# Optimization experiments

Hardware: AMD Instinct MI355X
Metric: run time of the kernel (lower is better)

## Reference

```python
import jax, jax.numpy as jnp
import numpy as np

P, N, M = 4, 8192, 8192

def setup_inputs() -> dict:
    key = jax.random.key(0)
    k1, k2, k3, k4, k5 = jax.random.split(key, 5)
    return {
        "camera_pts": jax.random.normal(k1, (P, N, 3), dtype=jnp.float32),
        "cad_pts": jax.random.normal(k2, (P, M, 3), dtype=jnp.float32),
        "part_weight": jax.random.uniform(k3, (P,), dtype=jnp.float32),
        "rot_quat": jax.random.normal(k4, (P, 4), dtype=jnp.float32),
        "tra": jax.random.normal(k5, (P, 3, 1), dtype=jnp.float32),
    }

def _quat_to_rot(q):
    # q: [P,4] in (w,x,y,z) order, normalized outside
    a, b, c, d = q[:, 0], q[:, 1], q[:, 2], q[:, 3]
    rows = jnp.stack([
        1 - 2*c*c - 2*d*d, 2*b*c - 2*a*d,     2*a*c + 2*b*d,
        2*b*c + 2*a*d,     1 - 2*b*b - 2*d*d, 2*c*d - 2*a*b,
        2*b*d - 2*a*c,     2*a*b + 2*c*d,     1 - 2*b*b - 2*c*c,
    ], axis=-1)  # [P,9]
    return rows.reshape(-1, 3, 3)

def _chamfer(x, y):
    # x: [N,4], y: [M,4] -> scalar bidirectional chamfer (Euclidean, not squared)
    x2 = jnp.sum(x * x, axis=-1)              # [N]
    y2 = jnp.sum(y * y, axis=-1)              # [M]
    d2 = x2[:, None] + y2[None, :] - 2.0 * (x @ y.T)
    dist = jnp.sqrt(jnp.clip(d2, 0.0))        # [N,M]
    return jnp.mean(jnp.min(dist, axis=1)) + jnp.mean(jnp.min(dist, axis=0))

def reference(camera_pts, cad_pts, part_weight, rot_quat, tra):
    q = rot_quat / jnp.linalg.norm(rot_quat, axis=1, keepdims=True)
    rot = _quat_to_rot(q)                                       # [P,3,3]
    top = jnp.concatenate([rot, tra], axis=2)                   # [P,3,4]
    bottom = jnp.broadcast_to(jnp.array([[[0.0, 0.0, 0.0, 1.0]]], dtype=rot.dtype), (rot.shape[0], 1, 4))
    transforms = jnp.concatenate([top, bottom], axis=1)         # [P,4,4]
    ones_cad = jnp.ones(cad_pts.shape[:-1] + (1,), dtype=cad_pts.dtype)
    ones_cam = jnp.ones(camera_pts.shape[:-1] + (1,), dtype=camera_pts.dtype)
    cad_h = jnp.concatenate([cad_pts, ones_cad], axis=-1)       # [P,M,4]
    cam_h = jnp.concatenate([camera_pts, ones_cam], axis=-1)    # [P,N,4]
    cad_base = jnp.einsum('pij,pmj->pmi', transforms, cad_h)    # [P,M,4]
    cd = jax.vmap(_chamfer)(cad_base, cam_h)                    # [P]
    all_objective = jnp.sum(part_weight * cd)
    return all_objective, jax.lax.stop_gradient(transforms)
```

## Files before the change

kernel.cpp:

```cpp
#include <hip/hip_runtime.h>
#include <math.h>

#define NP 4
#define NN 8192
#define NM 8192

#define PKA_OFF 0
#define PKB_OFF 131072
#define PRA_OFF 262144
#define PRB_OFF 393216
#define MINS_OFF 524288

#define TQ 8
#define QT 2048
#define SPLITS 64
#define SPAN 128

typedef float float2v __attribute__((ext_vector_type(2)));
typedef float float4v __attribute__((ext_vector_type(4)));

__device__ inline float min3f(float a, float b, float c) {
    float d;
    asm("v_min3_f32 %0, %1, %2, %3" : "=v"(d) : "v"(a), "v"(b), "v"(c));
    return d;
}

__device__ inline float2v pk_fma(float2v a, float2v b, float2v c) {
    float2v d;
    asm("v_pk_fma_f32 %0, %1, %2, %3" : "=v"(d) : "v"(a), "v"(b), "v"(c));
    return d;
}

__device__ inline void make_transform(const float* __restrict__ quat,
                                      const float* __restrict__ tra,
                                      int p, float T[12]) {
    float q0 = quat[p * 4 + 0], q1 = quat[p * 4 + 1];
    float q2 = quat[p * 4 + 2], q3 = quat[p * 4 + 3];
    float inv = 1.0f / sqrtf(q0 * q0 + q1 * q1 + q2 * q2 + q3 * q3);
    float a = q0 * inv, b = q1 * inv, c = q2 * inv, d = q3 * inv;
    T[0] = 1.0f - 2.0f * c * c - 2.0f * d * d;
    T[1] = 2.0f * b * c - 2.0f * a * d;
    T[2] = 2.0f * a * c + 2.0f * b * d;
    T[3] = tra[p * 3 + 0];
    T[4] = 2.0f * b * c + 2.0f * a * d;
    T[5] = 1.0f - 2.0f * b * b - 2.0f * d * d;
    T[6] = 2.0f * c * d - 2.0f * a * b;
    T[7] = tra[p * 3 + 1];
    T[8] = 2.0f * b * d - 2.0f * a * c;
    T[9] = 2.0f * a * b + 2.0f * c * d;
    T[10] = 1.0f - 2.0f * b * b - 2.0f * c * c;
    T[11] = tra[p * 3 + 2];
}

__global__ __launch_bounds__(256) void prep_kernel(
    const float* __restrict__ cam, const float* __restrict__ cad,
    const float* __restrict__ quat, const float* __restrict__ tra,
    float* __restrict__ ws, float* __restrict__ out) {
    int idx = blockIdx.x * 256 + threadIdx.x;

    float vx, vy, vz;
    int pkoff, proff, local;
    if (idx < NP * NM) {
        int p = idx >> 13;
        float T[12];
        make_transform(quat, tra, p, T);
        float x = cad[idx * 3 + 0];
        float y = cad[idx * 3 + 1];
        float z = cad[idx * 3 + 2];
        vx = fmaf(T[0], x, fmaf(T[1], y, fmaf(T[2], z, T[3])));
        vy = fmaf(T[4], x, fmaf(T[5], y, fmaf(T[6], z, T[7])));
        vz = fmaf(T[8], x, fmaf(T[9], y, fmaf(T[10], z, T[11])));
        pkoff = PKA_OFF;
        proff = PRA_OFF;
        local = idx;
    } else {
        int k = idx - NP * NM;
        vx = cam[k * 3 + 0];
        vy = cam[k * 3 + 1];
        vz = cam[k * 3 + 2];
        pkoff = PKB_OFF;
        proff = PRB_OFF;
        local = k;
    }
    float h = 0.5f * (vx * vx + vy * vy + vz * vz);
    ((float4*)(ws + pkoff))[local] = make_float4(vx, vy, vz, h);
    int lane = local & 1;
    size_t f = (size_t)proff + (size_t)(local & ~1) * 4;
    ws[f + lane] = vx;
    ws[f + 2 + lane] = vy;
    ws[f + 4 + lane] = vz;
    ws[f + 6 + lane] = h;

    if (idx < 64) {
        int p2 = idx >> 4;
        int r = (idx >> 2) & 3;
        int c = idx & 3;
        float T[12];
        make_transform(quat, tra, p2, T);
        float v;
        if (r == 3)
            v = (c == 3) ? 1.0f : 0.0f;
        else
            v = T[r * 4 + c];
        out[1 + idx] = v;
    } else if (idx == 64) {
        out[0] = 0.0f;
    }
}

__global__ __launch_bounds__(256)
__attribute__((amdgpu_waves_per_eu(2, 4)))
void chamfer_kernel(const float* __restrict__ ws, float* __restrict__ part) {
    int tid = threadIdx.x;
    int p = blockIdx.z >> 1;
    int role = blockIdx.z & 1;

    const float4* Q;
    const float4v* T;
    if (role == 0) {
        Q = (const float4*)(ws + PKA_OFF) + p * NM;
        T = (const float4v*)(ws + PRB_OFF) + p * NN;
    } else {
        Q = (const float4*)(ws + PKB_OFF) + p * NN;
        T = (const float4v*)(ws + PRA_OFF) + p * NM;
    }
    float* po = part + (((size_t)blockIdx.z * SPLITS + blockIdx.y) << 13);

    __shared__ float4v sQd[SPAN];

    const float INF = __uint_as_float(0x7f800000u);
    int q0 = blockIdx.x * QT + tid;
    float2v nqx[TQ], nqy[TQ], nqz[TQ];
    float qw[TQ], tmin[TQ];
#pragma unroll
    for (int k = 0; k < TQ; ++k) {
        float4 v = Q[q0 + k * 256];
        nqx[k] = (float2v){-v.x, -v.x};
        nqy[k] = (float2v){-v.y, -v.y};
        nqz[k] = (float2v){-v.z, -v.z};
        qw[k] = v.w;
        tmin[k] = INF;
    }

    int tbase = blockIdx.y * SPAN;
    if (tid < SPAN) sQd[tid] = T[tbase + tid];
    __syncthreads();

    float4v cXY = sQd[0], cZH = sQd[1];
#pragma unroll 2
    for (int pp = 0; pp < SPAN / 2; ++pp) {
        int pn = (pp + 1) & (SPAN / 2 - 1);
        float4v nXY = sQd[2 * pn];
        float4v nZH = sQd[2 * pn + 1];

        float2v X = __builtin_shufflevector(cXY, cXY, 0, 1);
        float2v Y = __builtin_shufflevector(cXY, cXY, 2, 3);
        float2v Z = __builtin_shufflevector(cZH, cZH, 0, 1);
        float2v H = __builtin_shufflevector(cZH, cZH, 2, 3);
#pragma unroll
        for (int k = 0; k < TQ; ++k) {
            float2v s = pk_fma(nqx[k], X, pk_fma(nqy[k], Y, pk_fma(nqz[k], Z, H)));
            tmin[k] = min3f(tmin[k], s.x, s.y);
        }
        cXY = nXY;
        cZH = nZH;
    }

#pragma unroll
    for (int k = 0; k < TQ; ++k) {
        float d2 = 2.0f * (qw[k] + tmin[k]);
        po[q0 + k * 256] = fmaxf(d2, 0.0f);
    }
}

__global__ __launch_bounds__(256) void finalize_kernel(
    const float* __restrict__ ws, const float* __restrict__ w,
    float* __restrict__ out) {
    const float* part = ws + MINS_OFF;
    int i = blockIdx.x * 256 + threadIdx.x;
    int tid = threadIdx.x;
    int z = i >> 13;
    int q = i & 8191;
    const float* base = part + ((size_t)z << 19) + q;

    float m0 = base[(size_t)0 << 13];
    float m1 = base[(size_t)1 << 13];
    float m2 = base[(size_t)2 << 13];
    float m3 = base[(size_t)3 << 13];
#pragma unroll
    for (int y = 4; y < SPLITS; y += 4) {
        m0 = fminf(m0, base[(size_t)(y + 0) << 13]);
        m1 = fminf(m1, base[(size_t)(y + 1) << 13]);
        m2 = fminf(m2, base[(size_t)(y + 2) << 13]);
        m3 = fminf(m3, base[(size_t)(y + 3) << 13]);
    }
    float m = fminf(fminf(m0, m1), fminf(m2, m3));

    float acc = w[z >> 1] * sqrtf(m);

#pragma unroll
    for (int off = 32; off > 0; off >>= 1) acc += __shfl_down(acc, off, 64);

    __shared__ float wsum[4];
    if ((tid & 63) == 0) wsum[tid >> 6] = acc;
    __syncthreads();
    if (tid == 0) {
        float blocksum = (wsum[0] + wsum[1] + wsum[2] + wsum[3]) * (1.0f / 8192.0f);
        atomicAdd(out, blocksum);
    }
}

extern "C" void kernel_launch(void* const* d_in, const int* in_sizes, int n_in,
                              void* d_out, int out_size, void* d_ws, size_t ws_size,
                              hipStream_t stream) {
    const float* cam = (const float*)d_in[0];
    const float* cad = (const float*)d_in[1];
    const float* w = (const float*)d_in[2];
    const float* quat = (const float*)d_in[3];
    const float* tra = (const float*)d_in[4];
    float* out = (float*)d_out;
    float* ws = (float*)d_ws;

    prep_kernel<<<256, 256, 0, stream>>>(cam, cad, quat, tra, ws, out);

    dim3 grid(NM / QT, SPLITS, 2 * NP);
    chamfer_kernel<<<grid, 256, 0, stream>>>(ws, ws + MINS_OFF);

    finalize_kernel<<<256, 256, 0, stream>>>(ws, w, out);
}
```

Baseline: 115.2 us.

## Fuse point transform prep into chamfer kernel and halve split count

Removes the separate prep kernel. Each chamfer block now reads the raw camera and CAD points, applies the quaternion transform and computes the half-norm itself, staging targets straight into shared memory. The transform output is also written from block zero. Splits drop from 64 to 32 with a 256-point span per block, which halves the partial-min buffer that finalize has to reduce and saves one kernel launch. The cost is redundant transform math and strided 12-byte loads in every block, plus fewer blocks in the grid.

```diff
diff --git a/kernel.cpp b/kernel.cpp
--- a/kernel.cpp
+++ b/kernel.cpp
@@ -5,16 +5,10 @@
 #define NN 8192
 #define NM 8192
 
-#define PKA_OFF 0
-#define PKB_OFF 131072
-#define PRA_OFF 262144
-#define PRB_OFF 393216
-#define MINS_OFF 524288
-
 #define TQ 8
 #define QT 2048
-#define SPLITS 64
-#define SPAN 128
+#define SPLITS 32
+#define SPAN 256
 
 typedef float float2v __attribute__((ext_vector_type(2)));
 typedef float float4v __attribute__((ext_vector_type(4)));
@@ -52,100 +46,85 @@
     T[11] = tra[p * 3 + 2];
 }
 
-__global__ __launch_bounds__(256) void prep_kernel(
-    const float* __restrict__ cam, const float* __restrict__ cad,
-    const float* __restrict__ quat, const float* __restrict__ tra,
-    float* __restrict__ ws, float* __restrict__ out) {
-    int idx = blockIdx.x * 256 + threadIdx.x;
-
-    float vx, vy, vz;
-    int pkoff, proff, local;
-    if (idx < NP * NM) {
-        int p = idx >> 13;
-        float T[12];
-        make_transform(quat, tra, p, T);
-        float x = cad[idx * 3 + 0];
-        float y = cad[idx * 3 + 1];
-        float z = cad[idx * 3 + 2];
-        vx = fmaf(T[0], x, fmaf(T[1], y, fmaf(T[2], z, T[3])));
-        vy = fmaf(T[4], x, fmaf(T[5], y, fmaf(T[6], z, T[7])));
-        vz = fmaf(T[8], x, fmaf(T[9], y, fmaf(T[10], z, T[11])));
-        pkoff = PKA_OFF;
-        proff = PRA_OFF;
-        local = idx;
-    } else {
-        int k = idx - NP * NM;
-        vx = cam[k * 3 + 0];
-        vy = cam[k * 3 + 1];
-        vz = cam[k * 3 + 2];
-        pkoff = PKB_OFF;
-        proff = PRB_OFF;
-        local = k;
-    }
-    float h = 0.5f * (vx * vx + vy * vy + vz * vz);
-    ((float4*)(ws + pkoff))[local] = make_float4(vx, vy, vz, h);
-    int lane = local & 1;
-    size_t f = (size_t)proff + (size_t)(local & ~1) * 4;
-    ws[f + lane] = vx;
-    ws[f + 2 + lane] = vy;
-    ws[f + 4 + lane] = vz;
-    ws[f + 6 + lane] = h;
-
-    if (idx < 64) {
-        int p2 = idx >> 4;
-        int r = (idx >> 2) & 3;
-        int c = idx & 3;
-        float T[12];
-        make_transform(quat, tra, p2, T);
-        float v;
-        if (r == 3)
-            v = (c == 3) ? 1.0f : 0.0f;
-        else
-            v = T[r * 4 + c];
-        out[1 + idx] = v;
-    } else if (idx == 64) {
-        out[0] = 0.0f;
-    }
-}
-
-__global__ __launch_bounds__(256)
-__attribute__((amdgpu_waves_per_eu(2, 4)))
-void chamfer_kernel(const float* __restrict__ ws, float* __restrict__ part) {
+__global__ __launch_bounds__(256, 4)
+void chamfer_kernel(const float* __restrict__ cam, const float* __restrict__ cad,
+                    const float* __restrict__ quat, const float* __restrict__ tra,
+                    float* __restrict__ part, float* __restrict__ out) {
     int tid = threadIdx.x;
     int p = blockIdx.z >> 1;
     int role = blockIdx.z & 1;
 
-    const float4* Q;
-    const float4v* T;
-    if (role == 0) {
-        Q = (const float4*)(ws + PKA_OFF) + p * NM;
-        T = (const float4v*)(ws + PRB_OFF) + p * NN;
-    } else {
-        Q = (const float4*)(ws + PKB_OFF) + p * NN;
-        T = (const float4v*)(ws + PRA_OFF) + p * NM;
-    }
-    float* po = part + (((size_t)blockIdx.z * SPLITS + blockIdx.y) << 13);
-
-    __shared__ float4v sQd[SPAN];
+    float T[12];
+    make_transform(quat, tra, p, T);
+
+    if (blockIdx.x == 0 && blockIdx.y == 0 && blockIdx.z == 0) {
+        if (tid < 64) {
+            int p2 = tid >> 4;
+            int r = (tid >> 2) & 3;
+            int c = tid & 3;
+            float T2[12];
+            make_transform(quat, tra, p2, T2);
+            float v;
+            if (r == 3)
+                v = (c == 3) ? 1.0f : 0.0f;
+            else
+                v = T2[r * 4 + c];
+            out[1 + tid] = v;
+        } else if (tid == 64) {
+            out[0] = 0.0f;
+        }
+    }
+
+    __shared__ float sQf[SPAN * 4];
+    {
+        int j = tid;
+        const float* src = (role ? cad : cam) +
+                           ((size_t)p * 8192 + blockIdx.y * SPAN + j) * 3;
+        float x = src[0], y = src[1], z = src[2];
+        float vx, vy, vz;
+        if (role) {
+            vx = fmaf(T[0], x, fmaf(T[1], y, fmaf(T[2], z, T[3])));
+            vy = fmaf(T[4], x, fmaf(T[5], y, fmaf(T[6], z, T[7])));
+            vz = fmaf(T[8], x, fmaf(T[9], y, fmaf(T[10], z, T[11])));
+        } else {
+            vx = x; vy = y; vz = z;
+        }
+        float h = 0.5f * (vx * vx + vy * vy + vz * vz);
+        int lane = j & 1;
+        int f = (j & ~1) * 4;
+        sQf[f + lane] = vx;
+        sQf[f + 2 + lane] = vy;
+        sQf[f + 4 + lane] = vz;
+        sQf[f + 6 + lane] = h;
+    }
 
     const float INF = __uint_as_float(0x7f800000u);
     int q0 = blockIdx.x * QT + tid;
+    const float* qbase = (role ? cam : cad) + (size_t)p * 8192 * 3;
     float2v nqx[TQ], nqy[TQ], nqz[TQ];
     float qw[TQ], tmin[TQ];
 #pragma unroll
     for (int k = 0; k < TQ; ++k) {
-        float4 v = Q[q0 + k * 256];
-        nqx[k] = (float2v){-v.x, -v.x};
-        nqy[k] = (float2v){-v.y, -v.y};
-        nqz[k] = (float2v){-v.z, -v.z};
-        qw[k] = v.w;
+        const float* s = qbase + (size_t)(q0 + k * 256) * 3;
+        float x = s[0], y = s[1], z = s[2];
+        float vx, vy, vz;
+        if (!role) {
+            vx = fmaf(T[0], x, fmaf(T[1], y, fmaf(T[2], z, T[3])));
+            vy = fmaf(T[4], x, fmaf(T[5], y, fmaf(T[6], z, T[7])));
+            vz = fmaf(T[8], x, fmaf(T[9], y, fmaf(T[10], z, T[11])));
+        } else {
+            vx = x; vy = y; vz = z;
+        }
+        float h = 0.5f * (vx * vx + vy * vy + vz * vz);
+        nqx[k] = (float2v){-vx, -vx};
+        nqy[k] = (float2v){-vy, -vy};
+        nqz[k] = (float2v){-vz, -vz};
+        qw[k] = h;
         tmin[k] = INF;
     }
-
-    int tbase = blockIdx.y * SPAN;
-    if (tid < SPAN) sQd[tid] = T[tbase + tid];
     __syncthreads();
 
+    const float4v* sQd = (const float4v*)sQf;
     float4v cXY = sQd[0], cZH = sQd[1];
 #pragma unroll 2
     for (int pp = 0; pp < SPAN / 2; ++pp) {
@@ -166,6 +145,7 @@
         cZH = nZH;
     }
 
+    float* po = part + (((size_t)blockIdx.z * SPLITS + blockIdx.y) << 13);
 #pragma unroll
     for (int k = 0; k < TQ; ++k) {
         float d2 = 2.0f * (qw[k] + tmin[k]);
@@ -174,14 +154,13 @@
 }
 
 __global__ __launch_bounds__(256) void finalize_kernel(
-    const float* __restrict__ ws, const float* __restrict__ w,
+    const float* __restrict__ part, const float* __restrict__ w,
     float* __restrict__ out) {
-    const float* part = ws + MINS_OFF;
     int i = blockIdx.x * 256 + threadIdx.x;
     int tid = threadIdx.x;
     int z = i >> 13;
     int q = i & 8191;
-    const float* base = part + ((size_t)z << 19) + q;
+    const float* base = part + ((size_t)z * SPLITS << 13) + q;
 
     float m0 = base[(size_t)0 << 13];
     float m1 = base[(size_t)1 << 13];
@@ -221,10 +200,8 @@
     float* out = (float*)d_out;
     float* ws = (float*)d_ws;
 
-    prep_kernel<<<256, 256, 0, stream>>>(cam, cad, quat, tra, ws, out);
-
     dim3 grid(NM / QT, SPLITS, 2 * NP);
-    chamfer_kernel<<<grid, 256, 0, stream>>>(ws, ws + MINS_OFF);
+    chamfer_kernel<<<grid, 256, 0, stream>>>(cam, cad, quat, tra, ws, out);
 
     finalize_kernel<<<256, 256, 0, stream>>>(ws, w, out);
 }
```

Result: faster. 108.0 us (-6.3%).
